# Kernel optimization log

Hardware: AMD Instinct MI355X
Metric: run time of the kernel (lower is better)

The kernel has to match this reference:

```python
import jax, jax.numpy as jnp
import numpy as np

CHUNK_SIZE = 2048
LOCAL_WINDOW = 384
CHUNK_LEN = CHUNK_SIZE - LOCAL_WINDOW  # 1664
N_HEADS = 16
N_KV_HEADS = 4
HEAD_DIM = 128
HIDDEN = 2048
SEQ = 3 * CHUNK_LEN  # 4992
NEG_INF = -1e9


def _cos_sin(positions, dim=HEAD_DIM, base=10000.0):
    inv = 1.0 / (base ** (np.arange(0, dim, 2, dtype=np.float64) / dim))
    freqs = np.outer(np.asarray(positions, np.float64), inv)
    emb = np.concatenate([freqs, freqs], axis=-1)
    return jnp.asarray(np.cos(emb), jnp.float32), jnp.asarray(np.sin(emb), jnp.float32)


def setup_inputs() -> dict:
    key = jax.random.key(0)
    ks = jax.random.split(key, 5)
    hidden_states = jax.random.normal(ks[0], (1, SEQ, HIDDEN), jnp.float32) * 0.02
    position_ids = jnp.arange(SEQ, dtype=jnp.int32)[None, :]
    q_cos, q_sin = _cos_sin(np.arange(SEQ))                 # intra rotary (positions mod chunk_len)
    qc_cos, qc_sin = _cos_sin(np.arange(SEQ) + CHUNK_LEN)   # cross-chunk rotary variant
    k_cos, k_sin = _cos_sin(np.arange(SEQ))                 # key rotary (absolute positions)
    kv_dim = N_KV_HEADS * HEAD_DIM
    Wq = jax.random.normal(ks[1], (N_HEADS * HEAD_DIM, HIDDEN), jnp.float32) * 0.02
    Wk = jax.random.normal(ks[2], (kv_dim, HIDDEN), jnp.float32) * 0.02
    Wv = jax.random.normal(ks[3], (kv_dim, HIDDEN), jnp.float32) * 0.02
    Wo = jax.random.normal(ks[4], (HIDDEN, N_HEADS * HEAD_DIM), jnp.float32) * 0.02
    return dict(hidden_states=hidden_states, position_ids=position_ids,
                q_cos=q_cos, q_sin=q_sin, qc_cos=qc_cos, qc_sin=qc_sin,
                k_cos=k_cos, k_sin=k_sin, Wq=Wq, Wk=Wk, Wv=Wv, Wo=Wo)


def _rotate_half(x):
    x1, x2 = jnp.split(x, 2, axis=-1)
    return jnp.concatenate([-x2, x1], axis=-1)


def _rope(x, cos_t, sin_t, pid):
    # x: [b,h,s,d], pid: [b,s] -> cos/sin [b,1,s,d]
    cos = cos_t[pid][:, None]
    sin = sin_t[pid][:, None]
    return x * cos + _rotate_half(x) * sin


def _attn(q, k, v, causal):
    # flash-attn semantics: scale = head_dim**-0.5, returns output and fp32 LSE [b,h,q]
    scale = q.shape[-1] ** -0.5
    s = jnp.einsum('bhqd,bhkd->bhqk', q, k).astype(jnp.float32) * scale
    if causal:
        L, K = s.shape[-2], s.shape[-1]
        mask = jnp.tril(jnp.ones((L, K), bool))
        s = jnp.where(mask, s, NEG_INF)
    lse = jax.nn.logsumexp(s, axis=-1)
    p = jax.nn.softmax(s, axis=-1).astype(q.dtype)
    out = jnp.einsum('bhqk,bhkd->bhqd', p, v)
    return out, lse


def _merge(parts):
    # LSE-weighted merge of partial attention outputs (weights detached, as in torch)
    outs = jnp.stack([p[0] for p in parts])       # [n,b,h,q,d]
    lses = jnp.stack([p[1] for p in parts])       # [n,b,h,q] fp32
    w = jax.lax.stop_gradient(jax.nn.softmax(lses, axis=0))
    return jnp.sum(outs * w[..., None].astype(outs.dtype), axis=0)


def _forward(hidden_states, position_ids, q_cos, q_sin, qc_cos, qc_sin, k_cos, k_sin, Wq, Wk, Wv, Wo):
    b, s, _ = hidden_states.shape
    q = (hidden_states @ Wq.T).reshape(b, s, N_HEADS, HEAD_DIM).transpose(0, 2, 1, 3)
    k = (hidden_states @ Wk.T).reshape(b, s, N_KV_HEADS, HEAD_DIM).transpose(0, 2, 1, 3)
    v = (hidden_states @ Wv.T).reshape(b, s, N_KV_HEADS, HEAD_DIM).transpose(0, 2, 1, 3)

    k = _rope(k, k_cos, k_sin, position_ids)
    pid = position_ids % CHUNK_LEN

    groups = N_HEADS // N_KV_HEADS
    k = jnp.repeat(k, groups, axis=1)
    v = jnp.repeat(v, groups, axis=1)

    n_chunks = s // CHUNK_LEN
    # chunk 0: intra causal only
    q0 = _rope(q[:, :, :CHUNK_LEN], q_cos, q_sin, pid[:, :CHUNK_LEN])
    out0, _ = _attn(q0, k[:, :, :CHUNK_LEN], v[:, :, :CHUNK_LEN], causal=True)
    outs = [out0]
    for i in range(1, n_chunks):
        b0 = i * CHUNK_LEN
        e = b0 + CHUNK_LEN
        qi = q[:, :, b0:e]
        pid_c = pid[:, b0:e]
        parts = [_attn(_rope(qi, q_cos, q_sin, pid_c), k[:, :, b0:e], v[:, :, b0:e], causal=True),
                 _attn(_rope(qi, qc_cos, qc_sin, pid_c), k[:, :, b0 - CHUNK_LEN:b0], v[:, :, b0 - CHUNK_LEN:b0], causal=False)]
        if b0 - CHUNK_LEN > 0:
            pid_i = jnp.full_like(pid_c, CHUNK_LEN - 1)
            parts.append(_attn(_rope(qi, qc_cos, qc_sin, pid_i), k[:, :, :b0 - CHUNK_LEN], v[:, :, :b0 - CHUNK_LEN], causal=False))
        outs.append(_merge(parts))
    attn_out = jnp.concatenate(outs, axis=2)                      # [b,h,s,d]
    attn_out = attn_out.transpose(0, 2, 1, 3).reshape(b, s, -1)   # [b,s,h*d]
    return attn_out @ Wo.T


def reference(hidden_states, position_ids, q_cos, q_sin, qc_cos, qc_sin, k_cos, k_sin, Wq, Wk, Wv, Wo):
    return _forward(hidden_states, position_ids, q_cos, q_sin, qc_cos, qc_sin, k_cos, k_sin, Wq, Wk, Wv, Wo)
```

## Files before the change

kernel.cpp:

```cpp
#include <hip/hip_runtime.h>

typedef unsigned short u16;
typedef unsigned int u32;
typedef __attribute__((ext_vector_type(8))) __bf16 bf16x8;
typedef __attribute__((ext_vector_type(4))) float f32x4;
typedef __attribute__((ext_vector_type(16))) float f32x16;

#define CLEN 1664
#define SEQL 4992
#define NHEADS 16
#define HD 128
#define HID 2048
#define KVD 512
#define SCALE 0.08838834764831845f
#define SCLOG2E 0.12752615142058843f
#define NHEAVY 48
#define NSMALL 36

__device__ __forceinline__ u16 f2bf(float f) {
  union { float f; u32 u; } v; v.f = f;
  u32 u = v.u;
  return (u16)((u + 0x7FFFu + ((u >> 16) & 1u)) >> 16);
}
__device__ __forceinline__ float bf2f(u16 h) {
  union { u32 u; float f; } v; v.u = (u32)h << 16;
  return v.f;
}
__device__ __forceinline__ f32x4 mfma16(bf16x8 a, bf16x8 b, f32x4 c) {
  return __builtin_amdgcn_mfma_f32_16x16x32_bf16(a, b, c, 0, 0, 0);
}
__device__ __forceinline__ f32x16 mfma32(bf16x8 a, bf16x8 b, f32x16 c) {
  return __builtin_amdgcn_mfma_f32_32x32x16_bf16(a, b, c, 0, 0, 0);
}
__device__ __forceinline__ u32 cvtpk(float lo, float hi) {
  u32 r;
  asm("v_cvt_pk_bf16_f32 %0, %1, %2" : "=v"(r) : "v"(lo), "v"(hi));
  return r;
}
__device__ __forceinline__ float exp2v(float x) {
  float r;
  asm("v_exp_f32 %0, %1" : "=v"(r) : "v"(x));
  return r;
}
__device__ __forceinline__ void gload_lds16(const u16* g, u16* l) {
  __builtin_amdgcn_global_load_lds((const __attribute__((address_space(1))) void*)g,
                                   (__attribute__((address_space(3))) void*)l, 16, 0, 0);
}

#define CVT_Q0 2555904
#define CVT_Q1 1048576
#define CVT_Q2 262144
#define CVT_Q3 262144
#define CVT_Q4 1048576
__device__ __forceinline__ void cvt4(const float* s, u16* d, int q) {
  float4 v = *(const float4*)(s + (size_t)q * 4);
  uint2 p;
  p.x = (u32)f2bf(v.x) | ((u32)f2bf(v.y) << 16);
  p.y = (u32)f2bf(v.z) | ((u32)f2bf(v.w) << 16);
  *(uint2*)(d + (size_t)q * 4) = p;
}
__global__ void cvt_all_kernel(const float* __restrict__ hidden, const float* __restrict__ Wq,
                               const float* __restrict__ Wk, const float* __restrict__ Wv,
                               const float* __restrict__ Wo, u16* __restrict__ h_bf,
                               u16* __restrict__ Wqkv, u16* __restrict__ Wo_bf,
                               u32* __restrict__ cnt) {
  int q = blockIdx.x * blockDim.x + threadIdx.x;
  if (q < 8) { cnt[q * 64] = 0; cnt[q * 64 + 1] = 0; }
  if (q < CVT_Q0) { cvt4(hidden, h_bf, q); return; }
  q -= CVT_Q0;
  if (q < CVT_Q1) { cvt4(Wq, Wqkv, q); return; }
  q -= CVT_Q1;
  if (q < CVT_Q2) { cvt4(Wk, Wqkv + 2048 * 2048, q); return; }
  q -= CVT_Q2;
  if (q < CVT_Q3) { cvt4(Wv, Wqkv + 2560 * 2048, q); return; }
  q -= CVT_Q3;
  if (q < CVT_Q4) cvt4(Wo, Wo_bf, q);
}

#define RP_N0 1277952
#define RP_N1 851968
#define RP_N2 425984
#define RP_N3 319488
__device__ __forceinline__ void rope8(const u16* __restrict__ src, u16* __restrict__ dst,
                                      const float* __restrict__ ctab, const float* __restrict__ stab,
                                      int s, int dstrow, int col, int rowlen, int pid, float scl) {
  const int dh = col & 127;
  const bool hih = dh >= 64;
  const u16* rowp = src + (size_t)s * rowlen;
  union { uint4 u; u16 h[8]; } X, P, O;
  X.u = *(const uint4*)(rowp + col);
  P.u = *(const uint4*)(rowp + col + (hih ? -64 : 64));
  const float* cp = ctab + pid * 128 + dh;
  const float* sp = stab + pid * 128 + dh;
#pragma unroll
  for (int j = 0; j < 8; ++j) {
    float v = bf2f(X.h[j]) * cp[j] + (hih ? bf2f(P.h[j]) : -bf2f(P.h[j])) * sp[j];
    O.h[j] = f2bf(v * scl);
  }
  *(uint4*)(dst + (size_t)dstrow * rowlen + col) = O.u;
}
__global__ void rope_all_kernel(const u16* __restrict__ q_tmp, const u16* __restrict__ k_tmp,
                                u16* __restrict__ qa, u16* __restrict__ qb, u16* __restrict__ qf,
                                u16* __restrict__ k_bf, const float* __restrict__ q_cos,
                                const float* __restrict__ q_sin, const float* __restrict__ qc_cos,
                                const float* __restrict__ qc_sin, const float* __restrict__ k_cos,
                                const float* __restrict__ k_sin) {
  int o = blockIdx.x * blockDim.x + threadIdx.x;
  if (o < RP_N0) {
    int r = o >> 8, col = (o & 255) * 8;
    rope8(q_tmp, qa, q_cos, q_sin, r, r, col, 2048, r % CLEN, SCLOG2E);
    return;
  }
  o -= RP_N0;
  if (o < RP_N1) {
    int r = o >> 8, col = (o & 255) * 8, s = CLEN + r;
    rope8(q_tmp, qb, qc_cos, qc_sin, s, r, col, 2048, s % CLEN, SCLOG2E);
    return;
  }
  o -= RP_N1;
  if (o < RP_N2) {
    int r = o >> 8, col = (o & 255) * 8, s = 2 * CLEN + r;
    rope8(q_tmp, qf, qc_cos, qc_sin, s, r, col, 2048, CLEN - 1, SCLOG2E);
    return;
  }
  o -= RP_N2;
  if (o < RP_N3) {
    int r = o >> 6, col = (o & 63) * 8;
    rope8(k_tmp, k_bf, k_cos, k_sin, r, r, col, 512, r, 1.0f);
  }
}

__global__ __launch_bounds__(256) void gemm_qkv(const u16* __restrict__ A, const u16* __restrict__ B,
                                                u16* __restrict__ q_tmp, u16* __restrict__ k_tmp,
                                                u16* __restrict__ vT) {
  __shared__ __align__(16) u16 Al[128 * 64];
  __shared__ __align__(16) u16 Bl[128 * 64];
  const int K = HID;
  const int t = threadIdx.x;
  const int lane = t & 63, wid = t >> 6;
  const int g = lane >> 4, c = lane & 15;
  const int wr = wid >> 1, wc = wid & 1;
  const int bid = blockIdx.x;
  const int wg = (bid & 7) * 117 + (bid >> 3);
  const int m0 = (wg % 39) * 128, n0 = (wg / 39) * 128;

  f32x4 acc[4][4];
#pragma unroll
  for (int m = 0; m < 4; ++m)
#pragma unroll
    for (int n = 0; n < 4; ++n) acc[m][n] = (f32x4){0.f, 0.f, 0.f, 0.f};

  const int scol = (t & 7) * 8;
  for (int k0 = 0; k0 < K; k0 += 64) {
    __syncthreads();
#pragma unroll
    for (int i = 0; i < 4; ++i) {
      const int r = i * 32 + (t >> 3);
      gload_lds16(A + (size_t)(m0 + r) * K + k0 + scol, Al + i * 2048 + wid * 512);
      gload_lds16(B + (size_t)(n0 + r) * K + k0 + scol, Bl + i * 2048 + wid * 512);
    }
    __syncthreads();
#pragma unroll
    for (int kk = 0; kk < 2; ++kk) {
      bf16x8 af[4], bfr[4];
#pragma unroll
      for (int m = 0; m < 4; ++m)
        af[m] = *(const bf16x8*)(Al + (wr * 64 + m * 16 + c) * 64 + kk * 32 + g * 8);
#pragma unroll
      for (int n = 0; n < 4; ++n)
        bfr[n] = *(const bf16x8*)(Bl + (wc * 64 + n * 16 + c) * 64 + kk * 32 + g * 8);
#pragma unroll
      for (int m = 0; m < 4; ++m)
#pragma unroll
        for (int n = 0; n < 4; ++n)
          acc[m][n] = mfma16(af[m], bfr[n], acc[m][n]);
    }
  }
#pragma unroll
  for (int m = 0; m < 4; ++m)
#pragma unroll
    for (int n = 0; n < 4; ++n)
#pragma unroll
      for (int j = 0; j < 4; ++j) {
        const int row = m0 + wr * 64 + m * 16 + 4 * g + j;
        const int col = n0 + wc * 64 + n * 16 + c;
        const float v = acc[m][n][j];
        if (n0 < 2048)       q_tmp[(size_t)row * 2048 + col] = f2bf(v);
        else if (n0 < 2560)  k_tmp[(size_t)row * 512 + (col - 2048)] = f2bf(v);
        else                 vT[(size_t)(col - 2560) * SEQL + row] = f2bf(v);
      }
}

__global__ __launch_bounds__(256) void gemm_o(const u16* __restrict__ A, const u16* __restrict__ B,
                                              float* __restrict__ Cf) {
  __shared__ __align__(16) u16 Al[128 * 64];
  __shared__ __align__(16) u16 Bl[128 * 64];
  const int K = HID, N = HID;
  const int t = threadIdx.x;
  const int lane = t & 63, wid = t >> 6;
  const int g = lane >> 4, c = lane & 15;
  const int wr = wid >> 1, wc = wid & 1;
  const int bid = blockIdx.x;
  const int wg = (bid & 7) * 78 + (bid >> 3);
  const int m0 = (wg % 39) * 128, n0 = (wg / 39) * 128;

  f32x4 acc[4][4];
#pragma unroll
  for (int m = 0; m < 4; ++m)
#pragma unroll
    for (int n = 0; n < 4; ++n) acc[m][n] = (f32x4){0.f, 0.f, 0.f, 0.f};

  const int scol = (t & 7) * 8;
  for (int k0 = 0; k0 < K; k0 += 64) {
    __syncthreads();
#pragma unroll
    for (int i = 0; i < 4; ++i) {
      const int r = i * 32 + (t >> 3);
      gload_lds16(A + (size_t)(m0 + r) * K + k0 + scol, Al + i * 2048 + wid * 512);
      gload_lds16(B + (size_t)(n0 + r) * K + k0 + scol, Bl + i * 2048 + wid * 512);
    }
    __syncthreads();
#pragma unroll
    for (int kk = 0; kk < 2; ++kk) {
      bf16x8 af[4], bfr[4];
#pragma unroll
      for (int m = 0; m < 4; ++m)
        af[m] = *(const bf16x8*)(Al + (wr * 64 + m * 16 + c) * 64 + kk * 32 + g * 8);
#pragma unroll
      for (int n = 0; n < 4; ++n)
        bfr[n] = *(const bf16x8*)(Bl + (wc * 64 + n * 16 + c) * 64 + kk * 32 + g * 8);
#pragma unroll
      for (int m = 0; m < 4; ++m)
#pragma unroll
        for (int n = 0; n < 4; ++n)
          acc[m][n] = mfma16(af[m], bfr[n], acc[m][n]);
    }
  }
#pragma unroll
  for (int m = 0; m < 4; ++m)
#pragma unroll
    for (int n = 0; n < 4; ++n)
#pragma unroll
      for (int j = 0; j < 4; ++j) {
        const int row = m0 + wr * 64 + m * 16 + 4 * g + j;
        const int col = n0 + wc * 64 + n * 16 + c;
        Cf[(size_t)row * N + col] = acc[m][n][j];
      }
}

__global__ __launch_bounds__(512, 4) void attn_kernel(
    const u16* __restrict__ qa, const u16* __restrict__ qbuf, const u16* __restrict__ qf,
    const u16* __restrict__ kbf, const u16* __restrict__ vT,
    u16* __restrict__ Opart, float* __restrict__ lseout, u32* __restrict__ cnt) {
  __shared__ __align__(16) u16 smem[2 * 16384];
  __shared__ int wsh;

  const int t = threadIdx.x, wid = t >> 6, lane = t & 63;
  const int ql = lane & 31, hi = lane >> 5;
  const int qid = blockIdx.x & 7;
  const int kvh = qid >> 1, headpar = qid & 1;
  const int ksr = t >> 4, ksc = t & 15;
  const int vsr = t >> 3, vsc = t & 7;

  for (;;) {
    __syncthreads();
    if (t == 0) {
      int h = (int)atomicAdd(cnt + qid * 64, 1u);
      if (h >= NHEAVY) {
        int s2 = (int)atomicAdd(cnt + qid * 64 + 1, 1u);
        h = (s2 < NSMALL) ? (NHEAVY + s2) : -1;
      }
      wsh = h;
    }
    __syncthreads();
    const int w = wsh;
    if (w < 0) break;

    const int head = kvh * 4 + ((w & 1) << 1) + headpar;
    const int rk = w >> 1;
    int chunk, seg, qb;
    if (rk < 21) {
      const int part = rk / 7; qb = rk % 7;
      chunk = (part == 0) ? 1 : 2;
      seg = (part == 2) ? 1 : 0;
    } else if (rk < 24) {
      chunk = rk - 21; seg = chunk; qb = 6;
    } else {
      const int g2 = rk - 24;
      qb = 5 - g2 / 3; chunk = g2 % 3; seg = chunk;
    }
    const bool causal = (seg == chunk);
    const int nt = causal ? ((qb == 6) ? 26 : (4 * qb + 4)) : 26;
    const int slot = causal ? 0 : ((chunk - seg == 1) ? 1 : 2);
    const int kvbase = seg * CLEN;
    const int qcb = qb * 256 + wid * 32;
    const int qpos = qcb + ql;
    const bool wact = qcb < CLEN;

    const u16* qp; int qoff;
    if (causal)                { qp = qa;   qoff = 0; }
    else if (chunk - seg == 1) { qp = qbuf; qoff = CLEN; }
    else                       { qp = qf;   qoff = 2 * CLEN; }

    bf16x8 aq[8];
    {
      const int qrow = wact ? (chunk * CLEN + qpos - qoff) : 0;
      const u16* qptr = qp + (size_t)qrow * HID + head * HD + hi * 8;
#pragma unroll
      for (int ck = 0; ck < 8; ++ck) aq[ck] = *(const bf16x8*)(qptr + ck * 16);
    }

    float l_r = 0.f;
    f32x16 oacc[4];
#pragma unroll
    for (int db = 0; db < 4; ++db)
#pragma unroll
      for (int r = 0; r < 16; ++r) oacc[db][r] = 0.f;

    auto stage = [&](int b, int kt) {
      const int kv0 = kt * 64;
#pragma unroll
      for (int i = 0; i < 2; ++i) {
        const int rr = ksr + 32 * i;
        const int gs = ksc ^ (rr & 7);
        gload_lds16(kbf + (size_t)(kvbase + kv0 + rr) * KVD + kvh * HD + gs * 8,
                    smem + b * 16384 + i * 4096 + wid * 512);
      }
#pragma unroll
      for (int i = 0; i < 2; ++i) {
        const int rr = vsr + 64 * i;
        const int gs = vsc ^ (rr & 7);
        gload_lds16(vT + (size_t)(kvh * HD + rr) * SEQL + kvbase + kv0 + gs * 8,
                    smem + b * 16384 + 8192 + i * 4096 + wid * 512);
      }
    };

    stage(0, 0);
    int cur = 0;
    for (int kt = 0; kt < nt; ++kt) {
      if (kt + 1 < nt) {
        stage(cur ^ 1, kt + 1);
        asm volatile("s_waitcnt vmcnt(4)" ::: "memory");
      } else {
        asm volatile("s_waitcnt vmcnt(0)" ::: "memory");
      }
      __builtin_amdgcn_s_barrier();
      const int kv0 = kt * 64;
      const u16* Kb = smem + cur * 16384;
      const u16* Vb = smem + cur * 16384 + 8192;
#pragma unroll
      for (int s = 0; s < 2; ++s) {
        if (wact && !(causal && kv0 + 32 * s > qcb + 31)) {
          f32x16 sacc;
#pragma unroll
          for (int r = 0; r < 16; ++r) sacc[r] = 0.f;
          const int kr = 32 * s + ql;
          const int r7 = lane & 7;
          __builtin_amdgcn_s_setprio(1);
#pragma unroll
          for (int ck = 0; ck < 8; ++ck) {
            bf16x8 kb = *(const bf16x8*)(Kb + kr * 128 + (((2 * ck + hi) ^ r7) * 8));
            sacc = mfma32(kb, aq[ck], sacc);
          }
          __builtin_amdgcn_s_setprio(0);
          const int thr = qpos - kv0 - 32 * s - 4 * hi;
          float e[16];
          float rs = 0.f;
#pragma unroll
          for (int r = 0; r < 16; ++r) {
            const int crow_r = (r & 3) + 8 * (r >> 2);
            float ev = (causal && crow_r > thr) ? -1e30f : sacc[r];
            e[r] = exp2v(ev);
            rs += e[r];
          }
          rs += __shfl_xor(rs, 32);
          l_r += rs;
          u32 wp[8];
#pragma unroll
          for (int j = 0; j < 8; ++j) wp[j] = cvtpk(e[2 * j], e[2 * j + 1]);
          __builtin_amdgcn_s_setprio(1);
#pragma unroll
          for (int ks = 0; ks < 2; ++ks) {
            union { uint4 u; bf16x8 v; } pa;
            pa.u.x = wp[4 * ks]; pa.u.y = wp[4 * ks + 1];
            pa.u.z = wp[4 * ks + 2]; pa.u.w = wp[4 * ks + 3];
            const int g4a = 8 * s + 4 * ks + hi;
            const int sw = (lane & 7) << 1;
#pragma unroll
            for (int db = 0; db < 4; ++db) {
              const int vrow = 32 * db + ql;
              const uint2 v0 = *(const uint2*)(Vb + vrow * 64 + ((g4a ^ sw) * 4));
              const uint2 v1 = *(const uint2*)(Vb + vrow * 64 + (((g4a + 2) ^ sw) * 4));
              union { uint4 u; bf16x8 v; } bv;
              bv.u.x = v0.x; bv.u.y = v0.y; bv.u.z = v1.x; bv.u.w = v1.y;
              oacc[db] = mfma32(pa.v, bv.v, oacc[db]);
            }
          }
          __builtin_amdgcn_s_setprio(0);
        }
      }
      __builtin_amdgcn_s_barrier();
      cur ^= 1;
    }
    if (wact) {
      const float linv = 1.0f / l_r;
      u16* scr = smem + wid * 4096;
#pragma unroll
      for (int r = 0; r < 16; ++r) {
        const int rrow = (r & 3) + 8 * (r >> 2) + 4 * hi;
        const float li = __shfl(linv, rrow);
#pragma unroll
        for (int db = 0; db < 4; ++db)
          scr[rrow * 128 + db * 32 + ql] = f2bf(oacc[db][r] * li);
      }
      asm volatile("s_waitcnt lgkmcnt(0)" ::: "memory");
      const int rcol = lane & 15;
#pragma unroll
      for (int p = 0; p < 8; ++p) {
        const int row = p * 4 + (lane >> 4);
        uint4 v = *(const uint4*)(scr + row * 128 + rcol * 8);
        const size_t grow = (size_t)(chunk * CLEN + qcb + row);
        *(uint4*)(Opart + ((size_t)slot * SEQL + grow) * HID + head * HD + rcol * 8) = v;
      }
      if (hi == 0)
        lseout[((size_t)slot * NHEADS + head) * SEQL + chunk * CLEN + qcb + ql] = __logf(l_r);
    }
  }
}

__global__ void merge_kernel(const u16* __restrict__ Opart, const float* __restrict__ lse,
                             u16* __restrict__ amrg) {
  const int idx = blockIdx.x * blockDim.x + threadIdx.x;
  const int row = idx >> 8;
  const int col = (idx & 255) * 8;
  const int head = col >> 7;
  const int np = row / CLEN + 1;
  float ls[3];
  float mx = -1e30f;
  for (int i = 0; i < np; ++i) {
    ls[i] = lse[((size_t)i * NHEADS + head) * SEQL + row];
    mx = fmaxf(mx, ls[i]);
  }
  float wsum = 0.f;
  for (int i = 0; i < np; ++i) { ls[i] = __expf(ls[i] - mx); wsum += ls[i]; }
  const float inv = 1.0f / wsum;
  float acc[8];
#pragma unroll
  for (int j = 0; j < 8; ++j) acc[j] = 0.f;
  for (int i = 0; i < np; ++i) {
    union { uint4 u; u16 h[8]; } X;
    X.u = *(const uint4*)(Opart + ((size_t)i * SEQL + row) * (size_t)HID + col);
#pragma unroll
    for (int j = 0; j < 8; ++j) acc[j] += ls[i] * bf2f(X.h[j]);
  }
  union { uint4 u; u16 h[8]; } O;
#pragma unroll
  for (int j = 0; j < 8; ++j) O.h[j] = f2bf(acc[j] * inv);
  *(uint4*)(amrg + (size_t)row * 2048 + col) = O.u;
}

extern "C" void kernel_launch(void* const* d_in, const int* in_sizes, int n_in,
                              void* d_out, int out_size, void* d_ws, size_t ws_size,
                              hipStream_t stream) {
  (void)in_sizes; (void)n_in; (void)out_size; (void)ws_size;
  const float* hidden = (const float*)d_in[0];
  const float* q_cos = (const float*)d_in[2];
  const float* q_sin = (const float*)d_in[3];
  const float* qc_cos = (const float*)d_in[4];
  const float* qc_sin = (const float*)d_in[5];
  const float* k_cos = (const float*)d_in[6];
  const float* k_sin = (const float*)d_in[7];
  const float* Wq = (const float*)d_in[8];
  const float* Wk = (const float*)d_in[9];
  const float* Wv = (const float*)d_in[10];
  const float* Wo = (const float*)d_in[11];
  float* out = (float*)d_out;

  char* ws = (char*)d_ws;
  u16* Wo_bf = (u16*)(ws + 0);
  u16* qa    = (u16*)(ws + 8388608);
  u16* qb    = (u16*)(ws + 28835840);
  u16* qf    = (u16*)(ws + 42467328);
  u16* k_bf  = (u16*)(ws + 49283072);
  u16* vT    = (u16*)(ws + 54394880);
  char* BIG  = ws + 59506688;
  u16* h_bf  = (u16*)(BIG + 0);
  u16* Wqkv  = (u16*)(BIG + 20447232);
  u16* q_tmp = (u16*)(BIG + 33030144);
  u16* k_tmp = (u16*)(BIG + 53477376);
  u16* Opart = (u16*)(BIG + 0);
  float* lse = (float*)(BIG + 61341696);
  u32* cnt   = (u32*)(BIG + 61341696 + 958464);
  u16* amrg  = qa;

  cvt_all_kernel<<<dim3(20224), dim3(256), 0, stream>>>(hidden, Wq, Wk, Wv, Wo, h_bf, Wqkv, Wo_bf, cnt);
  gemm_qkv<<<dim3(936), 256, 0, stream>>>(h_bf, Wqkv, q_tmp, k_tmp, vT);
  rope_all_kernel<<<dim3(11232), dim3(256), 0, stream>>>(q_tmp, k_tmp, qa, qb, qf, k_bf,
                                                         q_cos, q_sin, qc_cos, qc_sin, k_cos, k_sin);
  attn_kernel<<<dim3(512), dim3(512), 0, stream>>>(qa, qb, qf, k_bf, vT, Opart, lse, cnt);
  merge_kernel<<<dim3(SEQL), dim3(256), 0, stream>>>(Opart, lse, amrg);
  gemm_o<<<dim3(624), 256, 0, stream>>>(amrg, Wo_bf, out);
}
```

Baseline: 577.8 us.

## Replace persistent atomic work queue in attention with static one-block-per-tile grid

The attention kernel no longer runs persistent blocks that pull tiles from per-KV-head atomic counters. It now launches one block per work tile (672 blocks), decoding chunk, segment, query block and head directly from blockIdx, with heavy non-causal tiles first and causal tiles ordered by descending size. This removes the atomics, the extra barriers per tile and the counter reset in the convert kernel. In exchange it gives up the dynamic load balancing and the per-CU KV-head locality that the queue provided, leaving balance to the hardware block scheduler.

```diff
diff --git a/kernel.cpp b/kernel.cpp
--- a/kernel.cpp
+++ b/kernel.cpp
@@ -14,8 +14,6 @@
 #define KVD 512
 #define SCALE 0.08838834764831845f
 #define SCLOG2E 0.12752615142058843f
-#define NHEAVY 48
-#define NSMALL 36
 
 __device__ __forceinline__ u16 f2bf(float f) {
   union { float f; u32 u; } v; v.f = f;
@@ -62,10 +60,8 @@
 __global__ void cvt_all_kernel(const float* __restrict__ hidden, const float* __restrict__ Wq,
                                const float* __restrict__ Wk, const float* __restrict__ Wv,
                                const float* __restrict__ Wo, u16* __restrict__ h_bf,
-                               u16* __restrict__ Wqkv, u16* __restrict__ Wo_bf,
-                               u32* __restrict__ cnt) {
+                               u16* __restrict__ Wqkv, u16* __restrict__ Wo_bf) {
   int q = blockIdx.x * blockDim.x + threadIdx.x;
-  if (q < 8) { cnt[q * 64] = 0; cnt[q * 64 + 1] = 0; }
   if (q < CVT_Q0) { cvt4(hidden, h_bf, q); return; }
   q -= CVT_Q0;
   if (q < CVT_Q1) { cvt4(Wq, Wqkv, q); return; }
@@ -251,180 +247,164 @@
 __global__ __launch_bounds__(512, 4) void attn_kernel(
     const u16* __restrict__ qa, const u16* __restrict__ qbuf, const u16* __restrict__ qf,
     const u16* __restrict__ kbf, const u16* __restrict__ vT,
-    u16* __restrict__ Opart, float* __restrict__ lseout, u32* __restrict__ cnt) {
+    u16* __restrict__ Opart, float* __restrict__ lseout) {
   __shared__ __align__(16) u16 smem[2 * 16384];
-  __shared__ int wsh;
 
   const int t = threadIdx.x, wid = t >> 6, lane = t & 63;
   const int ql = lane & 31, hi = lane >> 5;
-  const int qid = blockIdx.x & 7;
-  const int kvh = qid >> 1, headpar = qid & 1;
   const int ksr = t >> 4, ksc = t & 15;
   const int vsr = t >> 3, vsc = t & 7;
 
-  for (;;) {
-    __syncthreads();
-    if (t == 0) {
-      int h = (int)atomicAdd(cnt + qid * 64, 1u);
-      if (h >= NHEAVY) {
-        int s2 = (int)atomicAdd(cnt + qid * 64 + 1, 1u);
-        h = (s2 < NSMALL) ? (NHEAVY + s2) : -1;
+  const int b = blockIdx.x;
+  int chunk, seg, qb, head;
+  if (b < 336) {
+    head = b & 15;
+    const int f = b >> 4;
+    const int part = f / 7; qb = f % 7;
+    chunk = (part == 0) ? 1 : 2;
+    seg = (part == 2) ? 1 : 0;
+  } else {
+    const int i = b - 336;
+    qb = 6 - i / 48;
+    const int j = i % 48;
+    head = j & 15; chunk = j >> 4; seg = chunk;
+  }
+  const bool causal = (seg == chunk);
+  const int nt = causal ? ((qb == 6) ? 26 : (4 * qb + 4)) : 26;
+  const int slot = causal ? 0 : ((chunk - seg == 1) ? 1 : 2);
+  const int kvh = head >> 2;
+  const int kvbase = seg * CLEN;
+  const int qcb = qb * 256 + wid * 32;
+  const int qpos = qcb + ql;
+  const bool wact = qcb < CLEN;
+
+  const u16* qp; int qoff;
+  if (causal)                { qp = qa;   qoff = 0; }
+  else if (chunk - seg == 1) { qp = qbuf; qoff = CLEN; }
+  else                       { qp = qf;   qoff = 2 * CLEN; }
+
+  bf16x8 aq[8];
+  {
+    const int qrow = wact ? (chunk * CLEN + qpos - qoff) : 0;
+    const u16* qptr = qp + (size_t)qrow * HID + head * HD + hi * 8;
+#pragma unroll
+    for (int ck = 0; ck < 8; ++ck) aq[ck] = *(const bf16x8*)(qptr + ck * 16);
+  }
+
+  float l_r = 0.f;
+  f32x16 oacc[4];
+#pragma unroll
+  for (int db = 0; db < 4; ++db)
+#pragma unroll
+    for (int r = 0; r < 16; ++r) oacc[db][r] = 0.f;
+
+  auto stage = [&](int bb, int kt) {
+    const int kv0 = kt * 64;
+#pragma unroll
+    for (int i = 0; i < 2; ++i) {
+      const int rr = ksr + 32 * i;
+      const int gs = ksc ^ (rr & 7);
+      gload_lds16(kbf + (size_t)(kvbase + kv0 + rr) * KVD + kvh * HD + gs * 8,
+                  smem + bb * 16384 + i * 4096 + wid * 512);
+    }
+#pragma unroll
+    for (int i = 0; i < 2; ++i) {
+      const int rr = vsr + 64 * i;
+      const int gs = vsc ^ (rr & 7);
+      gload_lds16(vT + (size_t)(kvh * HD + rr) * SEQL + kvbase + kv0 + gs * 8,
+                  smem + bb * 16384 + 8192 + i * 4096 + wid * 512);
+    }
+  };
+
+  stage(0, 0);
+  int cur = 0;
+  for (int kt = 0; kt < nt; ++kt) {
+    if (kt + 1 < nt) {
+      stage(cur ^ 1, kt + 1);
+      asm volatile("s_waitcnt vmcnt(4)" ::: "memory");
+    } else {
+      asm volatile("s_waitcnt vmcnt(0)" ::: "memory");
+    }
+    __builtin_amdgcn_s_barrier();
+    const int kv0 = kt * 64;
+    const u16* Kb = smem + cur * 16384;
+    const u16* Vb = smem + cur * 16384 + 8192;
+#pragma unroll
+    for (int s = 0; s < 2; ++s) {
+      if (wact && !(causal && kv0 + 32 * s > qcb + 31)) {
+        f32x16 sacc;
+#pragma unroll
+        for (int r = 0; r < 16; ++r) sacc[r] = 0.f;
+        const int kr = 32 * s + ql;
+        const int r7 = lane & 7;
+        __builtin_amdgcn_s_setprio(1);
+#pragma unroll
+        for (int ck = 0; ck < 8; ++ck) {
+          bf16x8 kb = *(const bf16x8*)(Kb + kr * 128 + (((2 * ck + hi) ^ r7) * 8));
+          sacc = mfma32(kb, aq[ck], sacc);
+        }
+        __builtin_amdgcn_s_setprio(0);
+        const int thr = qpos - kv0 - 32 * s - 4 * hi;
+        float e[16];
+        float rs = 0.f;
+#pragma unroll
+        for (int r = 0; r < 16; ++r) {
+          const int crow_r = (r & 3) + 8 * (r >> 2);
+          float ev = (causal && crow_r > thr) ? -1e30f : sacc[r];
+          e[r] = exp2v(ev);
+          rs += e[r];
+        }
+        rs += __shfl_xor(rs, 32);
+        l_r += rs;
+        u32 wp[8];
+#pragma unroll
+        for (int j = 0; j < 8; ++j) wp[j] = cvtpk(e[2 * j], e[2 * j + 1]);
+        __builtin_amdgcn_s_setprio(1);
+#pragma unroll
+        for (int ks = 0; ks < 2; ++ks) {
+          union { uint4 u; bf16x8 v; } pa;
+          pa.u.x = wp[4 * ks]; pa.u.y = wp[4 * ks + 1];
+          pa.u.z = wp[4 * ks + 2]; pa.u.w = wp[4 * ks + 3];
+          const int g4a = 8 * s + 4 * ks + hi;
+          const int sw = (lane & 7) << 1;
+#pragma unroll
+          for (int db = 0; db < 4; ++db) {
+            const int vrow = 32 * db + ql;
+            const uint2 v0 = *(const uint2*)(Vb + vrow * 64 + ((g4a ^ sw) * 4));
+            const uint2 v1 = *(const uint2*)(Vb + vrow * 64 + (((g4a + 2) ^ sw) * 4));
+            union { uint4 u; bf16x8 v; } bv;
+            bv.u.x = v0.x; bv.u.y = v0.y; bv.u.z = v1.x; bv.u.w = v1.y;
+            oacc[db] = mfma32(pa.v, bv.v, oacc[db]);
+          }
+        }
+        __builtin_amdgcn_s_setprio(0);
       }
-      wsh = h;
-    }
-    __syncthreads();
-    const int w = wsh;
-    if (w < 0) break;
-
-    const int head = kvh * 4 + ((w & 1) << 1) + headpar;
-    const int rk = w >> 1;
-    int chunk, seg, qb;
-    if (rk < 21) {
-      const int part = rk / 7; qb = rk % 7;
-      chunk = (part == 0) ? 1 : 2;
-      seg = (part == 2) ? 1 : 0;
-    } else if (rk < 24) {
-      chunk = rk - 21; seg = chunk; qb = 6;
-    } else {
-      const int g2 = rk - 24;
-      qb = 5 - g2 / 3; chunk = g2 % 3; seg = chunk;
-    }
-    const bool causal = (seg == chunk);
-    const int nt = causal ? ((qb == 6) ? 26 : (4 * qb + 4)) : 26;
-    const int slot = causal ? 0 : ((chunk - seg == 1) ? 1 : 2);
-    const int kvbase = seg * CLEN;
-    const int qcb = qb * 256 + wid * 32;
-    const int qpos = qcb + ql;
-    const bool wact = qcb < CLEN;
-
-    const u16* qp; int qoff;
-    if (causal)                { qp = qa;   qoff = 0; }
-    else if (chunk - seg == 1) { qp = qbuf; qoff = CLEN; }
-    else                       { qp = qf;   qoff = 2 * CLEN; }
-
-    bf16x8 aq[8];
-    {
-      const int qrow = wact ? (chunk * CLEN + qpos - qoff) : 0;
-      const u16* qptr = qp + (size_t)qrow * HID + head * HD + hi * 8;
-#pragma unroll
-      for (int ck = 0; ck < 8; ++ck) aq[ck] = *(const bf16x8*)(qptr + ck * 16);
-    }
-
-    float l_r = 0.f;
-    f32x16 oacc[4];
-#pragma unroll
-    for (int db = 0; db < 4; ++db)
-#pragma unroll
-      for (int r = 0; r < 16; ++r) oacc[db][r] = 0.f;
-
-    auto stage = [&](int b, int kt) {
-      const int kv0 = kt * 64;
-#pragma unroll
-      for (int i = 0; i < 2; ++i) {
-        const int rr = ksr + 32 * i;
-        const int gs = ksc ^ (rr & 7);
-        gload_lds16(kbf + (size_t)(kvbase + kv0 + rr) * KVD + kvh * HD + gs * 8,
-                    smem + b * 16384 + i * 4096 + wid * 512);
-      }
-#pragma unroll
-      for (int i = 0; i < 2; ++i) {
-        const int rr = vsr + 64 * i;
-        const int gs = vsc ^ (rr & 7);
-        gload_lds16(vT + (size_t)(kvh * HD + rr) * SEQL + kvbase + kv0 + gs * 8,
-                    smem + b * 16384 + 8192 + i * 4096 + wid * 512);
-      }
-    };
-
-    stage(0, 0);
-    int cur = 0;
-    for (int kt = 0; kt < nt; ++kt) {
-      if (kt + 1 < nt) {
-        stage(cur ^ 1, kt + 1);
-        asm volatile("s_waitcnt vmcnt(4)" ::: "memory");
-      } else {
-        asm volatile("s_waitcnt vmcnt(0)" ::: "memory");
-      }
-      __builtin_amdgcn_s_barrier();
-      const int kv0 = kt * 64;
-      const u16* Kb = smem + cur * 16384;
-      const u16* Vb = smem + cur * 16384 + 8192;
-#pragma unroll
-      for (int s = 0; s < 2; ++s) {
-        if (wact && !(causal && kv0 + 32 * s > qcb + 31)) {
-          f32x16 sacc;
-#pragma unroll
-          for (int r = 0; r < 16; ++r) sacc[r] = 0.f;
-          const int kr = 32 * s + ql;
-          const int r7 = lane & 7;
-          __builtin_amdgcn_s_setprio(1);
-#pragma unroll
-          for (int ck = 0; ck < 8; ++ck) {
-            bf16x8 kb = *(const bf16x8*)(Kb + kr * 128 + (((2 * ck + hi) ^ r7) * 8));
-            sacc = mfma32(kb, aq[ck], sacc);
-          }
-          __builtin_amdgcn_s_setprio(0);
-          const int thr = qpos - kv0 - 32 * s - 4 * hi;
-          float e[16];
-          float rs = 0.f;
-#pragma unroll
-          for (int r = 0; r < 16; ++r) {
-            const int crow_r = (r & 3) + 8 * (r >> 2);
-            float ev = (causal && crow_r > thr) ? -1e30f : sacc[r];
-            e[r] = exp2v(ev);
-            rs += e[r];
-          }
-          rs += __shfl_xor(rs, 32);
-          l_r += rs;
-          u32 wp[8];
-#pragma unroll
-          for (int j = 0; j < 8; ++j) wp[j] = cvtpk(e[2 * j], e[2 * j + 1]);
-          __builtin_amdgcn_s_setprio(1);
-#pragma unroll
-          for (int ks = 0; ks < 2; ++ks) {
-            union { uint4 u; bf16x8 v; } pa;
-            pa.u.x = wp[4 * ks]; pa.u.y = wp[4 * ks + 1];
-            pa.u.z = wp[4 * ks + 2]; pa.u.w = wp[4 * ks + 3];
-            const int g4a = 8 * s + 4 * ks + hi;
-            const int sw = (lane & 7) << 1;
-#pragma unroll
-            for (int db = 0; db < 4; ++db) {
-              const int vrow = 32 * db + ql;
-              const uint2 v0 = *(const uint2*)(Vb + vrow * 64 + ((g4a ^ sw) * 4));
-              const uint2 v1 = *(const uint2*)(Vb + vrow * 64 + (((g4a + 2) ^ sw) * 4));
-              union { uint4 u; bf16x8 v; } bv;
-              bv.u.x = v0.x; bv.u.y = v0.y; bv.u.z = v1.x; bv.u.w = v1.y;
-              oacc[db] = mfma32(pa.v, bv.v, oacc[db]);
-            }
-          }
-          __builtin_amdgcn_s_setprio(0);
-        }
-      }
-      __builtin_amdgcn_s_barrier();
-      cur ^= 1;
-    }
-    if (wact) {
-      const float linv = 1.0f / l_r;
-      u16* scr = smem + wid * 4096;
-#pragma unroll
-      for (int r = 0; r < 16; ++r) {
-        const int rrow = (r & 3) + 8 * (r >> 2) + 4 * hi;
-        const float li = __shfl(linv, rrow);
-#pragma unroll
-        for (int db = 0; db < 4; ++db)
-          scr[rrow * 128 + db * 32 + ql] = f2bf(oacc[db][r] * li);
-      }
-      asm volatile("s_waitcnt lgkmcnt(0)" ::: "memory");
-      const int rcol = lane & 15;
-#pragma unroll
-      for (int p = 0; p < 8; ++p) {
-        const int row = p * 4 + (lane >> 4);
-        uint4 v = *(const uint4*)(scr + row * 128 + rcol * 8);
-        const size_t grow = (size_t)(chunk * CLEN + qcb + row);
-        *(uint4*)(Opart + ((size_t)slot * SEQL + grow) * HID + head * HD + rcol * 8) = v;
-      }
-      if (hi == 0)
-        lseout[((size_t)slot * NHEADS + head) * SEQL + chunk * CLEN + qcb + ql] = __logf(l_r);
-    }
+    }
+    __builtin_amdgcn_s_barrier();
+    cur ^= 1;
+  }
+  if (wact) {
+    const float linv = 1.0f / l_r;
+    u16* scr = smem + wid * 4096;
+#pragma unroll
+    for (int r = 0; r < 16; ++r) {
+      const int rrow = (r & 3) + 8 * (r >> 2) + 4 * hi;
+      const float li = __shfl(linv, rrow);
+#pragma unroll
+      for (int db = 0; db < 4; ++db)
+        scr[rrow * 128 + db * 32 + ql] = f2bf(oacc[db][r] * li);
+    }
+    asm volatile("s_waitcnt lgkmcnt(0)" ::: "memory");
+    const int rcol = lane & 15;
+#pragma unroll
+    for (int p = 0; p < 8; ++p) {
+      const int row = p * 4 + (lane >> 4);
+      uint4 v = *(const uint4*)(scr + row * 128 + rcol * 8);
+      const size_t grow = (size_t)(chunk * CLEN + qcb + row);
+      *(uint4*)(Opart + ((size_t)slot * SEQL + grow) * HID + head * HD + rcol * 8) = v;
+    }
+    if (hi == 0)
+      lseout[((size_t)slot * NHEADS + head) * SEQL + chunk * CLEN + qcb + ql] = __logf(l_r);
   }
 }
 
@@ -490,14 +470,13 @@
   u16* k_tmp = (u16*)(BIG + 53477376);
   u16* Opart = (u16*)(BIG + 0);
   float* lse = (float*)(BIG + 61341696);
-  u32* cnt   = (u32*)(BIG + 61341696 + 958464);
   u16* amrg  = qa;
 
-  cvt_all_kernel<<<dim3(20224), dim3(256), 0, stream>>>(hidden, Wq, Wk, Wv, Wo, h_bf, Wqkv, Wo_bf, cnt);
+  cvt_all_kernel<<<dim3(20224), dim3(256), 0, stream>>>(hidden, Wq, Wk, Wv, Wo, h_bf, Wqkv, Wo_bf);
   gemm_qkv<<<dim3(936), 256, 0, stream>>>(h_bf, Wqkv, q_tmp, k_tmp, vT);
   rope_all_kernel<<<dim3(11232), dim3(256), 0, stream>>>(q_tmp, k_tmp, qa, qb, qf, k_bf,
                                                          q_cos, q_sin, qc_cos, qc_sin, k_cos, k_sin);
-  attn_kernel<<<dim3(512), dim3(512), 0, stream>>>(qa, qb, qf, k_bf, vT, Opart, lse, cnt);
+  attn_kernel<<<dim3(672), dim3(512), 0, stream>>>(qa, qb, qf, k_bf, vT, Opart, lse);
   merge_kernel<<<dim3(SEQL), dim3(256), 0, stream>>>(Opart, lse, amrg);
   gemm_o<<<dim3(624), 256, 0, stream>>>(amrg, Wo_bf, out);
 }
```

Result: faster. 502.1 us (-13.1%).
